# Kernel tuning notes

Measured on AMD Instinct MI355X. Metric: run time of the kernel, lower is better.

Reference implementation:

```python
import jax, jax.numpy as jnp
import numpy as np

BITS = 8
EPS = 1e-5
NUM_HEADS = 16


def quantize_weight(w, eps=EPS):
    # per-tensor abs-mean scale, ternary weights in {-1, 0, 1}
    scale = jnp.maximum(jnp.mean(jnp.abs(w)), eps)
    qw = jnp.clip(jnp.round(w / scale), -1.0, 1.0)
    return qw, scale


def bitlinear158_inference(x, qw, scale, bias=None, bits=BITS, eps=EPS):
    # per-token abs-max activation quantization to [-Q, Q-1]
    q = float(2 ** (bits - 1))
    gamma = jnp.maximum(jnp.max(jnp.abs(x), axis=-1, keepdims=True), eps)
    qx = jnp.clip(jnp.round(x * (q / gamma)), -q, q - 1.0)
    out = jnp.einsum('...i,oi->...o', qx, qw)
    out = out * (scale * gamma / q)
    if bias is not None:
        out = out + bias
    return out


def setup_inputs() -> dict:
    rng = jax.random.key(0)
    ks = jax.random.split(rng, 7)
    B, L, E = 4, 2048, 1024
    return {
        'query': jax.random.normal(ks[0], (B, L, E), jnp.float32),
        'key': jax.random.normal(ks[1], (B, L, E), jnp.float32),
        'value': jax.random.normal(ks[2], (B, L, E), jnp.float32),
        'in_proj_weight': jax.random.normal(ks[3], (3 * E, E), jnp.float32) * 0.02,
        'in_proj_bias': jax.random.normal(ks[4], (3 * E,), jnp.float32) * 0.02,
        'out_proj_weight': jax.random.normal(ks[5], (E, E), jnp.float32) * 0.02,
        'out_proj_bias': jax.random.normal(ks[6], (E,), jnp.float32) * 0.02,
    }


def reference(query, key, value, in_proj_weight, in_proj_bias, out_proj_weight, out_proj_bias):
    B, Lq, E = query.shape
    Lk = key.shape[1]
    H = NUM_HEADS
    D = E // H

    # quantize weights as done at __init__ time
    qw, kw, vw = jnp.split(in_proj_weight, 3, axis=0)  # each [E, E]
    qb, kb, vb = jnp.split(in_proj_bias, 3, axis=0)
    q_qw, q_s = quantize_weight(qw)
    k_qw, k_s = quantize_weight(kw)
    v_qw, v_s = quantize_weight(vw)
    o_qw, o_s = quantize_weight(out_proj_weight)

    # quantized projections [B, L, E]
    q = bitlinear158_inference(query, q_qw, q_s, qb)
    k = bitlinear158_inference(key, k_qw, k_s, kb)
    v = bitlinear158_inference(value, v_qw, v_s, vb)

    # [B, H, L, D]
    q = q.reshape(B, Lq, H, D).transpose(0, 2, 1, 3)
    k = k.reshape(B, Lk, H, D).transpose(0, 2, 1, 3)
    v = v.reshape(B, Lk, H, D).transpose(0, 2, 1, 3)

    scores = jnp.einsum('bhqd,bhkd->bhqk', q, k) / jnp.sqrt(jnp.asarray(D, q.dtype))
    attn = jax.nn.softmax(scores, axis=-1)
    ctx = jnp.einsum('bhqk,bhkd->bhqd', attn, v)  # [B, H, Lq, D]
    ctx = ctx.transpose(0, 2, 1, 3).reshape(B, Lq, E)

    out = bitlinear158_inference(ctx, o_qw, o_s, out_proj_bias)
    return out
```

## Files before the change

### kernel.cpp

```cpp
#include <hip/hip_runtime.h>
#include <cstdint>
#include <cstddef>

#define BB 4
#define LL 2048
#define EE 1024
#define HH 16
#define DD 64
#define TT (BB*LL)
#define EPSF 1e-5f

typedef _Float16 half8 __attribute__((ext_vector_type(8)));
typedef _Float16 half4v __attribute__((ext_vector_type(4)));
typedef float floatx4 __attribute__((ext_vector_type(4)));
typedef float floatx16 __attribute__((ext_vector_type(16)));
typedef int intx4 __attribute__((ext_vector_type(4)));
typedef unsigned int uintx4 __attribute__((ext_vector_type(4)));
typedef unsigned int uint2v __attribute__((ext_vector_type(2)));

__device__ __forceinline__ void gl_lds16(const void* g, void* l) {
    __builtin_amdgcn_global_load_lds(
        (const __attribute__((address_space(1))) void*)g,
        (__attribute__((address_space(3))) void*)l, 16, 0, 0);
}

__device__ __forceinline__ uint32_t pk2(float a, float b) {
    union { _Float16 h[2]; uint32_t u; } x;
    x.h[0] = (_Float16)a; x.h[1] = (_Float16)b;
    return x.u;
}

__device__ __forceinline__ uint32_t pkrtz(float a, float b) {
    return __builtin_bit_cast(uint32_t, __builtin_amdgcn_cvt_pkrtz(a, b));
}

__global__ void k_absum(const float* __restrict__ in_proj,
                        const float* __restrict__ out_proj,
                        double* __restrict__ sums) {
    const int which = blockIdx.y;
    const float* src = (which < 3) ? (in_proj + (size_t)which * EE * EE) : out_proj;
    double loc = 0.0;
    const int n = EE * EE;
    for (int i = blockIdx.x * blockDim.x + threadIdx.x; i < n; i += gridDim.x * blockDim.x)
        loc += (double)fabsf(src[i]);
    #pragma unroll
    for (int off = 32; off > 0; off >>= 1) loc += __shfl_down(loc, off, 64);
    __shared__ double red[4];
    const int lane = threadIdx.x & 63, wv = threadIdx.x >> 6;
    if (lane == 0) red[wv] = loc;
    __syncthreads();
    if (threadIdx.x == 0) {
        double tot = red[0] + red[1] + red[2] + red[3];
        atomicAdd(&sums[which], tot);
    }
}

__global__ void k_quantw(const float* __restrict__ in_proj,
                         const float* __restrict__ out_proj,
                         const double* __restrict__ sums,
                         float* __restrict__ scaleF,
                         int8_t* __restrict__ qw) {
    const int idx = blockIdx.x * blockDim.x + threadIdx.x;
    if (idx < 4) scaleF[idx] = fmaxf((float)(sums[idx] * (1.0 / (EE * EE))), EPSF);
    const int which = idx >> 20;
    const float s = fmaxf((float)(sums[which] * (1.0 / (EE * EE))), EPSF);
    const float w = (which < 3) ? in_proj[idx] : out_proj[idx - 3 * EE * EE];
    float q = rintf(w / s);
    q = fminf(fmaxf(q, -1.f), 1.f);
    qw[idx] = (int8_t)q;
}

__device__ __forceinline__ void gammaq_body(const float* __restrict__ x,
                                            float* __restrict__ g,
                                            int8_t* __restrict__ qx) {
    const int wv = threadIdx.x >> 6, lane = threadIdx.x & 63;
    const int tok = blockIdx.x * 4 + wv;
    const float* xp = x + (size_t)tok * EE;
    float4 v[4];
    #pragma unroll
    for (int i = 0; i < 4; i++) v[i] = *(const float4*)(xp + (lane + 64 * i) * 4);
    float m = 0.f;
    #pragma unroll
    for (int i = 0; i < 4; i++)
        m = fmaxf(m, fmaxf(fmaxf(fabsf(v[i].x), fabsf(v[i].y)),
                           fmaxf(fabsf(v[i].z), fabsf(v[i].w))));
    #pragma unroll
    for (int off = 1; off < 64; off <<= 1) m = fmaxf(m, __shfl_xor(m, off, 64));
    const float gg = fmaxf(m, EPSF);
    const float rg = 128.f / gg;
    int8_t* qp = qx + (size_t)tok * EE;
    #pragma unroll
    for (int i = 0; i < 4; i++) {
        char4 c;
        c.x = (int8_t)(int)fminf(fmaxf(rintf(v[i].x * rg), -128.f), 127.f);
        c.y = (int8_t)(int)fminf(fmaxf(rintf(v[i].y * rg), -128.f), 127.f);
        c.z = (int8_t)(int)fminf(fmaxf(rintf(v[i].z * rg), -128.f), 127.f);
        c.w = (int8_t)(int)fminf(fmaxf(rintf(v[i].w * rg), -128.f), 127.f);
        *(char4*)(qp + (lane + 64 * i) * 4) = c;
    }
    if (lane == 0) g[tok] = gg;
}

__global__ __launch_bounds__(256) void k_gammaq3(const float* __restrict__ q,
                                                 const float* __restrict__ k,
                                                 const float* __restrict__ v,
                                                 float* __restrict__ g,
                                                 int8_t* __restrict__ qx) {
    const int y = blockIdx.y;
    const float* src = (y == 0) ? q : (y == 1) ? k : v;
    gammaq_body(src, g + (size_t)y * TT, qx + (size_t)y * TT * EE);
}

__global__ __launch_bounds__(256) void k_gammaq(const float* __restrict__ x,
                                                float* __restrict__ g,
                                                int8_t* __restrict__ qx) {
    gammaq_body(x, g, qx);
}

__global__ __launch_bounds__(256) void k_bitmm(
    const int8_t* __restrict__ qx_all, const float* __restrict__ gam_all,
    const int8_t* __restrict__ qw_all, const float* __restrict__ scaleF,
    const float* __restrict__ in_proj_b, const float* __restrict__ out_proj_b,
    float* __restrict__ outF, _Float16* __restrict__ outH_all,
    int wbase, float qpre) {
    __shared__ __align__(16) int8_t smem[36864];
    int8_t (*As)[128] = (int8_t(*)[128])smem;
    int8_t (*Bs)[128] = (int8_t(*)[128])(smem + 16384);
    _Float16 (*Vt)[136] = (_Float16(*)[136])smem;
    const int widx = wbase + blockIdx.z;
    const int8_t* qx = qx_all + (size_t)widx * TT * EE;
    const int8_t* qw = qw_all + (size_t)widx * EE * EE;
    const float* gam = gam_all + (size_t)widx * TT;
    const float* bias = (widx < 3) ? (in_proj_b + widx * EE) : out_proj_b;
    _Float16* outH = outH_all + (size_t)widx * TT * EE;
    const float pre = (widx == 0) ? qpre : 1.0f;
    const int tid = threadIdx.x;
    const int wv = tid >> 6, lane = tid & 63;
    const int quad = lane >> 4, l16 = lane & 15;
    const int wm = wv & 1, wn = wv >> 1;
    const int t0 = blockIdx.x * 128, o0 = blockIdx.y * 128;
    const int srow = lane >> 3, schunk = lane & 7;

    intx4 acc[4][4];
    #pragma unroll
    for (int i = 0; i < 4; i++)
        #pragma unroll
        for (int j = 0; j < 4; j++) acc[i][j] = (intx4){0, 0, 0, 0};

    for (int k0 = 0; k0 < EE; k0 += 128) {
        __syncthreads();
        #pragma unroll
        for (int p = 0; p < 4; p++) {
            const int g = wv * 4 + p;
            const int c = schunk ^ srow ^ (g & 7);
            const int row = g * 8 + srow;
            gl_lds16(qx + (size_t)(t0 + row) * EE + k0 + c * 16, &As[g * 8][0]);
            gl_lds16(qw + (size_t)(o0 + row) * EE + k0 + c * 16, &Bs[g * 8][0]);
        }
        __syncthreads();
        #pragma unroll
        for (int kk = 0; kk < 2; kk++) {
            intx4 af[4], bf[4];
            #pragma unroll
            for (int s4 = 0; s4 < 4; s4++) {
                const int mR = (l16 & 7) ^ ((s4 * 2 + (l16 >> 3)) & 7);
                const int ph = ((kk * 4 + quad) ^ mR) * 16;
                af[s4] = *(const intx4*)&As[wm * 64 + s4 * 16 + l16][ph];
                bf[s4] = *(const intx4*)&Bs[wn * 64 + s4 * 16 + l16][ph];
            }
            #pragma unroll
            for (int sm = 0; sm < 4; sm++)
                #pragma unroll
                for (int sn = 0; sn < 4; sn++)
                    acc[sm][sn] = __builtin_amdgcn_mfma_i32_16x16x64_i8(
                        af[sm], bf[sn], acc[sm][sn], 0, 0, 0);
        }
    }

    const float s = scaleF[widx];
    if (widx == 2) {
        __syncthreads();
        #pragma unroll
        for (int sm = 0; sm < 4; sm++) {
            const int tl = wm * 64 + sm * 16 + quad * 4;
            float mr[4];
            #pragma unroll
            for (int r = 0; r < 4; r++) mr[r] = s * gam[t0 + tl + r] * 0.0078125f;
            #pragma unroll
            for (int sn = 0; sn < 4; sn++) {
                const int ol = wn * 64 + sn * 16 + l16;
                const float b = bias[o0 + ol];
                half4v hv;
                #pragma unroll
                for (int r = 0; r < 4; r++)
                    hv[r] = (_Float16)((float)acc[sm][sn][r] * mr[r] + b);
                *(half4v*)&Vt[ol][tl] = hv;
            }
        }
        __syncthreads();
        const int ol2 = tid >> 1, tc0 = (tid & 1) * 64;
        const int og = o0 + ol2, hh = og >> 6, dd = og & 63;
        const int bb = t0 >> 11, l0 = t0 & (LL - 1);
        _Float16* dst = outH + ((size_t)(bb * HH + hh) * DD + dd) * LL + l0 + tc0;
        #pragma unroll
        for (int i = 0; i < 8; i++)
            *(half8*)(dst + i * 8) = *(const half8*)&Vt[ol2][tc0 + i * 8];
        return;
    }
    #pragma unroll
    for (int sm = 0; sm < 4; sm++) {
        #pragma unroll
        for (int r = 0; r < 4; r++) {
            const int t = t0 + wm * 64 + sm * 16 + quad * 4 + r;
            const float mr = s * gam[t] * 0.0078125f;
            const int b_ = t >> 11, l_ = t & (LL - 1);
            #pragma unroll
            for (int sn = 0; sn < 4; sn++) {
                const int o = o0 + wn * 64 + sn * 16 + l16;
                const float val = (float)acc[sm][sn][r] * mr + bias[o];
                if (widx == 3) {
                    outF[(size_t)t * EE + o] = val;
                } else {
                    const int h_ = o >> 6, d_ = o & 63;
                    outH[((size_t)(b_ * HH + h_) * LL + l_) * DD + d_] = (_Float16)(val * pre);
                }
            }
        }
    }
}

__global__ __launch_bounds__(256, 4) void k_attn5(const _Float16* __restrict__ Q,
                                                  const _Float16* __restrict__ K,
                                                  const _Float16* __restrict__ Vt,
                                                  float* __restrict__ ctx) {
    __shared__ __align__(16) _Float16 Ksh[2][64][64];
    __shared__ __align__(16) _Float16 Vtsh[2][64][64];
    const int tid = threadIdx.x;
    const int wv = tid >> 6, lane = tid & 63;
    const int l32 = lane & 31, h2 = lane >> 5;
    const int bid = blockIdx.x;
    const int xcd = bid & 7, j = bid >> 3;
    const int bh = (xcd << 3) | (j >> 4);
    const int qblk = j & 15;
    const int b_ = bh >> 4, h_ = bh & 15;
    const int q0 = qblk * 128 + wv * 32;
    const int srow = lane >> 3, schunk = lane & 7;

    const _Float16* Qb = Q + (size_t)bh * LL * DD;
    const _Float16* Kb = K + (size_t)bh * LL * DD;
    const _Float16* Vtb = Vt + (size_t)bh * DD * LL;

    half8 qf[4];
    #pragma unroll
    for (int ds = 0; ds < 4; ds++)
        qf[ds] = *(const half8*)(Qb + (size_t)(q0 + l32) * DD + ds * 16 + h2 * 8);

    floatx16 acc[2], accl, zv;
    #pragma unroll
    for (int r = 0; r < 16; r++) { acc[0][r] = 0.f; acc[1][r] = 0.f; accl[r] = 0.f; zv[r] = 0.f; }
    half8 ones;
    #pragma unroll
    for (int r = 0; r < 8; r++) ones[r] = (_Float16)1.0f;

    {
        #pragma unroll
        for (int u = 0; u < 2; u++) {
            const int g = wv * 2 + u;
            const int c = schunk ^ srow ^ (g & 7);
            const int row = g * 8 + srow;
            gl_lds16(Kb + (size_t)row * DD + c * 8, &Ksh[0][g * 8][0]);
            gl_lds16(Vtb + (size_t)row * LL + c * 8, &Vtsh[0][g * 8][0]);
        }
    }
    __syncthreads();

    for (int kt = 0; kt < LL; kt += 64) {
        const int cur = (kt >> 6) & 1;

        if (kt + 64 < LL) {
            const int nkt = kt + 64;
            #pragma unroll
            for (int u = 0; u < 2; u++) {
                const int g = wv * 2 + u;
                const int c = schunk ^ srow ^ (g & 7);
                const int row = g * 8 + srow;
                gl_lds16(Kb + (size_t)(nkt + row) * DD + c * 8, &Ksh[cur ^ 1][g * 8][0]);
                gl_lds16(Vtb + (size_t)row * LL + nkt + c * 8, &Vtsh[cur ^ 1][g * 8][0]);
            }
        }

        half8 pa[4];
        #pragma unroll
        for (int ks = 0; ks < 2; ks++) {
            const int rowK = ks * 32 + l32;
            const int mK = (l32 & 7) ^ ((ks * 4 + (l32 >> 3)) & 7);
            __builtin_amdgcn_s_setprio(1);
            floatx16 sc;
            {
                const half8 kf = *(const half8*)&Ksh[cur][rowK][((2 * 0 + h2) ^ mK) * 8];
                sc = __builtin_amdgcn_mfma_f32_32x32x16_f16(kf, qf[0], zv, 0, 0, 0);
            }
            #pragma unroll
            for (int ds = 1; ds < 4; ds++) {
                const half8 kf = *(const half8*)&Ksh[cur][rowK][((2 * ds + h2) ^ mK) * 8];
                sc = __builtin_amdgcn_mfma_f32_32x32x16_f16(kf, qf[ds], sc, 0, 0, 0);
            }
            __builtin_amdgcn_s_setprio(0);
            float p[16];
            #pragma unroll
            for (int r = 0; r < 16; r++) p[r] = __builtin_amdgcn_exp2f(sc[r]);
            uint32_t u_[4][2];
            #pragma unroll
            for (int c4 = 0; c4 < 4; c4++) {
                u_[c4][0] = pkrtz(p[4 * c4 + 0], p[4 * c4 + 1]);
                u_[c4][1] = pkrtz(p[4 * c4 + 2], p[4 * c4 + 3]);
            }
            #pragma unroll
            for (int mm = 0; mm < 2; mm++) {
                uint2v s0 = __builtin_amdgcn_permlane32_swap(
                    u_[2 * mm][0], u_[2 * mm + 1][0], false, false);
                uint2v s1 = __builtin_amdgcn_permlane32_swap(
                    u_[2 * mm][1], u_[2 * mm + 1][1], false, false);
                uintx4 w;
                w[0] = s0[0]; w[1] = s1[0]; w[2] = s0[1]; w[3] = s1[1];
                union { uintx4 u; half8 h; } cv; cv.u = w;
                pa[ks * 2 + mm] = cv.h;
            }
        }

        __builtin_amdgcn_s_setprio(1);
        #pragma unroll
        for (int kb = 0; kb < 4; kb++) {
            #pragma unroll
            for (int sd = 0; sd < 2; sd++) {
                const int rowV = sd * 32 + l32;
                const int mV = (l32 & 7) ^ ((sd * 4 + (l32 >> 3)) & 7);
                const half8 vf = *(const half8*)&Vtsh[cur][rowV][((2 * kb + h2) ^ mV) * 8];
                acc[sd] = __builtin_amdgcn_mfma_f32_32x32x16_f16(pa[kb], vf, acc[sd], 0, 0, 0);
            }
            accl = __builtin_amdgcn_mfma_f32_32x32x16_f16(pa[kb], ones, accl, 0, 0, 0);
        }
        __builtin_amdgcn_s_setprio(0);

        __syncthreads();
    }

    #pragma unroll
    for (int r = 0; r < 16; r++) {
        const int qrow = (r & 3) + 8 * (r >> 2) + 4 * h2;
        const float iv = 1.f / accl[r];
        float* cp = ctx + ((size_t)b_ * LL + q0 + qrow) * EE + h_ * DD + l32;
        cp[0]  = acc[0][r] * iv;
        cp[32] = acc[1][r] * iv;
    }
}

extern "C" void kernel_launch(void* const* d_in, const int* in_sizes, int n_in,
                              void* d_out, int out_size, void* d_ws, size_t ws_size,
                              hipStream_t stream) {
    const float* query      = (const float*)d_in[0];
    const float* key        = (const float*)d_in[1];
    const float* value      = (const float*)d_in[2];
    const float* in_proj_w  = (const float*)d_in[3];
    const float* in_proj_b  = (const float*)d_in[4];
    const float* out_proj_w = (const float*)d_in[5];
    const float* out_proj_b = (const float*)d_in[6];
    float* out = (float*)d_out;

    char* ws = (char*)d_ws;
    double*   sums   = (double*)ws;
    float*    scaleF = (float*)(ws + 32);
    float*    gbuf   = (float*)(ws + 256);
    int8_t*   qw8    = (int8_t*)(ws + (size_t)1  * 1024 * 1024);
    int8_t*   qx8    = (int8_t*)(ws + (size_t)8  * 1024 * 1024);
    _Float16* Qh     = (_Float16*)(ws + (size_t)40 * 1024 * 1024);
    _Float16* Kh     = Qh + (size_t)TT * EE;
    _Float16* Vth    = Kh + (size_t)TT * EE;
    float*    ctx    = out;

    const float QPRE = 0.18033688011112042f;

    hipMemsetAsync(sums, 0, 32, stream);
    k_absum<<<dim3(64, 4), 256, 0, stream>>>(in_proj_w, out_proj_w, sums);
    k_quantw<<<(4 * EE * EE) / 256, 256, 0, stream>>>(in_proj_w, out_proj_w, sums, scaleF, qw8);
    k_gammaq3<<<dim3(TT / 4, 3), 256, 0, stream>>>(query, key, value, gbuf, qx8);

    k_bitmm<<<dim3(TT / 128, EE / 128, 3), 256, 0, stream>>>(
        qx8, gbuf, qw8, scaleF, in_proj_b, out_proj_b, nullptr, Qh, 0, QPRE);

    k_attn5<<<dim3((LL / 128) * BB * HH), 256, 0, stream>>>(Qh, Kh, Vth, ctx);

    k_gammaq<<<TT / 4, 256, 0, stream>>>(ctx, gbuf + 3 * TT, qx8 + 3 * (size_t)TT * EE);
    k_bitmm<<<dim3(TT / 128, EE / 128, 1), 256, 0, stream>>>(
        qx8, gbuf, qw8, scaleF, in_proj_b, out_proj_b, out, Qh, 3, QPRE);
}
```

Measured before the change: 340.5 us.

## Double-buffer int8 GEMM LDS tiles, remap blocks per XCD, vectorize absum

The int8 bit-GEMM now double-buffers its A/B tiles in 64KB of LDS, issuing the next k-slice's global-to-LDS loads before the MFMAs on the current slice, with one barrier per iteration. Wave priority is raised around the MFMA block. The grid is flattened to 1D and block ids are remapped so that consecutive token tiles land on the same XCD, which is meant to improve L2 reuse of shared qx rows. The weight abs-sum kernel uses float4 loads and a larger grid. Using 64KB of LDS lowers occupancy, which is the main risk.

```diff
diff --git a/kernel.cpp b/kernel.cpp
--- a/kernel.cpp
+++ b/kernel.cpp
@@ -24,12 +24,6 @@
         (__attribute__((address_space(3))) void*)l, 16, 0, 0);
 }
 
-__device__ __forceinline__ uint32_t pk2(float a, float b) {
-    union { _Float16 h[2]; uint32_t u; } x;
-    x.h[0] = (_Float16)a; x.h[1] = (_Float16)b;
-    return x.u;
-}
-
 __device__ __forceinline__ uint32_t pkrtz(float a, float b) {
     return __builtin_bit_cast(uint32_t, __builtin_amdgcn_cvt_pkrtz(a, b));
 }
@@ -38,11 +32,15 @@
                         const float* __restrict__ out_proj,
                         double* __restrict__ sums) {
     const int which = blockIdx.y;
-    const float* src = (which < 3) ? (in_proj + (size_t)which * EE * EE) : out_proj;
+    const float4* src = (const float4*)((which < 3) ? (in_proj + (size_t)which * EE * EE)
+                                                    : out_proj);
     double loc = 0.0;
-    const int n = EE * EE;
-    for (int i = blockIdx.x * blockDim.x + threadIdx.x; i < n; i += gridDim.x * blockDim.x)
-        loc += (double)fabsf(src[i]);
+    const int n4 = EE * EE / 4;
+    for (int i = blockIdx.x * blockDim.x + threadIdx.x; i < n4; i += gridDim.x * blockDim.x) {
+        const float4 v = src[i];
+        loc += (double)fabsf(v.x); loc += (double)fabsf(v.y);
+        loc += (double)fabsf(v.z); loc += (double)fabsf(v.w);
+    }
     #pragma unroll
     for (int off = 32; off > 0; off >>= 1) loc += __shfl_down(loc, off, 64);
     __shared__ double red[4];
@@ -123,11 +121,22 @@
     const float* __restrict__ in_proj_b, const float* __restrict__ out_proj_b,
     float* __restrict__ outF, _Float16* __restrict__ outH_all,
     int wbase, float qpre) {
-    __shared__ __align__(16) int8_t smem[36864];
-    int8_t (*As)[128] = (int8_t(*)[128])smem;
-    int8_t (*Bs)[128] = (int8_t(*)[128])(smem + 16384);
+    __shared__ __align__(16) int8_t smem[65536];
     _Float16 (*Vt)[136] = (_Float16(*)[136])smem;
-    const int widx = wbase + blockIdx.z;
+
+    const int nz = (wbase == 0) ? 3 : 1;
+    const int bid = blockIdx.x;
+    const int xcd = bid & 7;
+    const int idx = bid >> 3;
+    const int per = 8 * nz;
+    const int xl = idx / per;
+    const int rem = idx - xl * per;
+    const int y = rem & 7;
+    const int z = rem >> 3;
+    const int t0 = (xcd * 8 + xl) * 128;
+    const int o0 = y * 128;
+    const int widx = wbase + z;
+
     const int8_t* qx = qx_all + (size_t)widx * TT * EE;
     const int8_t* qw = qw_all + (size_t)widx * EE * EE;
     const float* gam = gam_all + (size_t)widx * TT;
@@ -138,7 +147,6 @@
     const int wv = tid >> 6, lane = tid & 63;
     const int quad = lane >> 4, l16 = lane & 15;
     const int wm = wv & 1, wn = wv >> 1;
-    const int t0 = blockIdx.x * 128, o0 = blockIdx.y * 128;
     const int srow = lane >> 3, schunk = lane & 7;
 
     intx4 acc[4][4];
@@ -147,17 +155,35 @@
         #pragma unroll
         for (int j = 0; j < 4; j++) acc[i][j] = (intx4){0, 0, 0, 0};
 
+    #pragma unroll
+    for (int p = 0; p < 4; p++) {
+        const int g = wv * 4 + p;
+        const int c = schunk ^ srow ^ (g & 7);
+        const int row = g * 8 + srow;
+        gl_lds16(qx + (size_t)(t0 + row) * EE + c * 16, smem + (size_t)(g * 8) * 128);
+        gl_lds16(qw + (size_t)(o0 + row) * EE + c * 16, smem + 32768 + (size_t)(g * 8) * 128);
+    }
+    __syncthreads();
+
     for (int k0 = 0; k0 < EE; k0 += 128) {
-        __syncthreads();
-        #pragma unroll
-        for (int p = 0; p < 4; p++) {
-            const int g = wv * 4 + p;
-            const int c = schunk ^ srow ^ (g & 7);
-            const int row = g * 8 + srow;
-            gl_lds16(qx + (size_t)(t0 + row) * EE + k0 + c * 16, &As[g * 8][0]);
-            gl_lds16(qw + (size_t)(o0 + row) * EE + k0 + c * 16, &Bs[g * 8][0]);
-        }
-        __syncthreads();
+        const int cur = (k0 >> 7) & 1;
+        int8_t (*As)[128] = (int8_t(*)[128])(smem + cur * 16384);
+        int8_t (*Bs)[128] = (int8_t(*)[128])(smem + 32768 + cur * 16384);
+
+        if (k0 + 128 < EE) {
+            int8_t* Asn = smem + (cur ^ 1) * 16384;
+            int8_t* Bsn = smem + 32768 + (cur ^ 1) * 16384;
+            const int kn = k0 + 128;
+            #pragma unroll
+            for (int p = 0; p < 4; p++) {
+                const int g = wv * 4 + p;
+                const int c = schunk ^ srow ^ (g & 7);
+                const int row = g * 8 + srow;
+                gl_lds16(qx + (size_t)(t0 + row) * EE + kn + c * 16, Asn + (size_t)(g * 8) * 128);
+                gl_lds16(qw + (size_t)(o0 + row) * EE + kn + c * 16, Bsn + (size_t)(g * 8) * 128);
+            }
+        }
+
         #pragma unroll
         for (int kk = 0; kk < 2; kk++) {
             intx4 af[4], bf[4];
@@ -168,18 +194,20 @@
                 af[s4] = *(const intx4*)&As[wm * 64 + s4 * 16 + l16][ph];
                 bf[s4] = *(const intx4*)&Bs[wn * 64 + s4 * 16 + l16][ph];
             }
+            __builtin_amdgcn_s_setprio(1);
             #pragma unroll
             for (int sm = 0; sm < 4; sm++)
                 #pragma unroll
                 for (int sn = 0; sn < 4; sn++)
                     acc[sm][sn] = __builtin_amdgcn_mfma_i32_16x16x64_i8(
                         af[sm], bf[sn], acc[sm][sn], 0, 0, 0);
-        }
+            __builtin_amdgcn_s_setprio(0);
+        }
+        __syncthreads();
     }
 
     const float s = scaleF[widx];
     if (widx == 2) {
-        __syncthreads();
         #pragma unroll
         for (int sm = 0; sm < 4; sm++) {
             const int tl = wm * 64 + sm * 16 + quad * 4;
@@ -381,16 +409,16 @@
     const float QPRE = 0.18033688011112042f;
 
     hipMemsetAsync(sums, 0, 32, stream);
-    k_absum<<<dim3(64, 4), 256, 0, stream>>>(in_proj_w, out_proj_w, sums);
+    k_absum<<<dim3(256, 4), 256, 0, stream>>>(in_proj_w, out_proj_w, sums);
     k_quantw<<<(4 * EE * EE) / 256, 256, 0, stream>>>(in_proj_w, out_proj_w, sums, scaleF, qw8);
     k_gammaq3<<<dim3(TT / 4, 3), 256, 0, stream>>>(query, key, value, gbuf, qx8);
 
-    k_bitmm<<<dim3(TT / 128, EE / 128, 3), 256, 0, stream>>>(
+    k_bitmm<<<dim3(64 * 8 * 3), 256, 0, stream>>>(
         qx8, gbuf, qw8, scaleF, in_proj_b, out_proj_b, nullptr, Qh, 0, QPRE);
 
     k_attn5<<<dim3((LL / 128) * BB * HH), 256, 0, stream>>>(Qh, Kh, Vth, ctx);
 
     k_gammaq<<<TT / 4, 256, 0, stream>>>(ctx, gbuf + 3 * TT, qx8 + 3 * (size_t)TT * EE);
-    k_bitmm<<<dim3(TT / 128, EE / 128, 1), 256, 0, stream>>>(
+    k_bitmm<<<dim3(64 * 8), 256, 0, stream>>>(
         qx8, gbuf, qw8, scaleF, in_proj_b, out_proj_b, out, Qh, 3, QPRE);
 }
```

Result: no change. 333.9 us (-1.9%).
